# Kernel tuning notes

Measured on AMD Instinct MI355X. Metric: run time of the kernel, lower is better.

## Reference

```python
import jax, jax.numpy as jnp
import numpy as np

B, L, E, H = 8, 2048, 1024, 16
D = E // H
EPS = 1e-6


def setup_inputs() -> dict:
    key = jax.random.key(0)
    ks = jax.random.split(key, 9)
    s = 1.0 / np.sqrt(E)
    def lin_w(k):
        return jax.random.uniform(k, (E, E), jnp.float32, -s, s)
    def lin_b(k):
        return jax.random.uniform(k, (E,), jnp.float32, -s, s)
    return {
        "query": jax.random.normal(ks[0], (B, L, E), jnp.float32),
        "Wq": lin_w(ks[1]), "bq": lin_b(ks[2]),
        "Wk": lin_w(ks[3]), "bk": lin_b(ks[4]),
        "Wv": lin_w(ks[5]), "bv": lin_b(ks[6]),
        "Wo": lin_w(ks[7]), "bo": lin_b(ks[8]),
    }


def reference(query, Wq, bq, Wk, bk, Wv, bv, Wo, bo):
    bsz, tgt_len, embed_dim = query.shape
    n_head = H
    head_dim = embed_dim // n_head
    m = tgt_len  # src_len == tgt_len (self-attention)

    # projections (torch Linear with W stored as (in, out) here)
    q = query @ Wq + bq
    k = query @ Wk + bk
    v = query @ Wv + bv

    # (B, L, E) -> (B, H, L, D), softmax feature map over head dim
    def to_heads(x):
        return x.reshape(bsz, tgt_len, n_head, head_dim).transpose(0, 2, 1, 3)

    q = jax.nn.softmax(to_heads(q), axis=-1)
    k = jax.nn.softmax(to_heads(k), axis=-1)
    v = to_heads(v)
    comp_q = 1.0 - q
    comp_k = 1.0 - k

    # cosFormer positional reweighting: idx = (pi/2) * (1..m) / m
    idx = (np.pi / 2) * jnp.arange(1, m + 1, dtype=jnp.float32) / m  # (L,)
    sin = jnp.sin(idx)[None, None, :, None]  # (1,1,L,1)
    cos = jnp.cos(idx)[None, None, :, None]

    def feat(x):  # (B,H,L,D) -> (B,H,L,2D)
        return jnp.concatenate([x * sin, x * cos], axis=-1)

    qf, comp_qf = feat(q), feat(comp_q)
    kf, comp_kf = feat(k), feat(comp_k)

    def branch(qf_, kf_):
        kv = jnp.einsum('bhld,bhlm->bhdm', kf_, v)            # (B,H,2D,D)
        z = 1.0 / jnp.maximum(
            jnp.einsum('bhld,bhd->bhl', qf_, kf_.sum(axis=2)), EPS)
        return jnp.einsum('bhld,bhdm,bhl->bhlm', qf_, kv, z)  # (B,H,L,D)

    attn = branch(qf, kf) + branch(comp_qf, comp_kf)

    # torch: (B*H,L,D).transpose(0,1).view(L,B,E)
    out = attn.transpose(2, 0, 1, 3).reshape(tgt_len, bsz, embed_dim)
    out = out @ Wo + bo
    # torch final: .view(bsz, tgt_len, n_feat) -- raw reshape, no transpose
    return out.reshape(bsz, tgt_len, embed_dim)
```

## Files before the change

### kernel.cpp

```cpp
#include <hip/hip_runtime.h>
#include <hip/hip_bf16.h>
#include <cstdint>

#define B_   8
#define L_   2048
#define E_   1024
#define H_   16
#define D_   64
#define M_   (B_ * L_)
#define EPS_ 1e-6f
#define PI2_ 1.57079632679f

typedef __bf16 bf16;
typedef __bf16 bf16x8 __attribute__((ext_vector_type(8)));
typedef __bf16 bf16x4 __attribute__((ext_vector_type(4)));
typedef float  floatx4 __attribute__((ext_vector_type(4)));

__device__ inline void async_cp16(const void* g, void* l) {
  __builtin_amdgcn_global_load_lds(
      (__attribute__((address_space(1))) void*)const_cast<void*>(g),
      (__attribute__((address_space(3))) void*)l,
      16, 0, 0);
}

__global__ __launch_bounds__(256) void k_convert_x(const float* __restrict__ x,
                                                   bf16* __restrict__ o) {
  size_t i = ((size_t)blockIdx.x * 256 + threadIdx.x) * 8;
  floatx4 a = *(const floatx4*)(x + i);
  floatx4 b = *(const floatx4*)(x + i + 4);
  bf16x8 r;
  r[0] = (bf16)a[0]; r[1] = (bf16)a[1]; r[2] = (bf16)a[2]; r[3] = (bf16)a[3];
  r[4] = (bf16)b[0]; r[5] = (bf16)b[1]; r[6] = (bf16)b[2]; r[7] = (bf16)b[3];
  *(bf16x8*)(o + i) = r;
}

struct TArgs { const float* src[4]; bf16* dst[4]; };

__global__ __launch_bounds__(256) void k_transpose_w(TArgs t) {
  __shared__ float tile[32][33];
  const float* src = t.src[blockIdx.z];
  bf16* dst = t.dst[blockIdx.z];
  int bx = blockIdx.x, by = blockIdx.y;
  int x = threadIdx.x, y = threadIdx.y;
#pragma unroll
  for (int i = 0; i < 4; i++) {
    int r = by * 32 + y + i * 8;
    tile[y + i * 8][x] = src[(size_t)r * E_ + bx * 32 + x];
  }
  __syncthreads();
#pragma unroll
  for (int i = 0; i < 4; i++) {
    int r = bx * 32 + y + i * 8;
    dst[(size_t)r * E_ + by * 32 + x] = (bf16)tile[x][y + i * 8];
  }
}

__global__ __launch_bounds__(256) void k_gemm_qkv(const bf16* __restrict__ A,
                                                  const bf16* __restrict__ Wt,
                                                  const float* __restrict__ bq,
                                                  const float* __restrict__ bk,
                                                  const float* __restrict__ bv,
                                                  float* __restrict__ QT,
                                                  float* __restrict__ KT,
                                                  bf16* __restrict__ VT) {
  __shared__ __attribute__((aligned(16))) bf16 As[128 * 32];
  __shared__ __attribute__((aligned(16))) bf16 Bs[128 * 32];
  const int id = blockIdx.x;
  const int bn = id & 7;
  const int q  = id >> 3;
  const int bm = q / 3;
  const int z  = q - bm * 3;
  const bf16* Bt = Wt + (size_t)z * E_ * E_;
  const float* bias = (z == 0) ? bq : (z == 1) ? bk : bv;

  const int tid  = threadIdx.x;
  const int wid  = tid >> 6;
  const int lane = tid & 63;
  const int quad = lane >> 4;
  const int l15  = lane & 15;
  const int wm   = wid >> 1, wn = wid & 1;

  const bf16* ga0 = A  + (size_t)(bm * 128 + wid * 32 + (lane >> 2)) * E_ + (lane & 3) * 8;
  const bf16* ga1 = ga0 + (size_t)16 * E_;
  const bf16* gb0 = Bt + (size_t)(bn * 128 + wid * 32 + (lane >> 2)) * E_ + (lane & 3) * 8;
  const bf16* gb1 = gb0 + (size_t)16 * E_;
  bf16* la = &As[wid * 1024];
  bf16* lb = &Bs[wid * 1024];

  floatx4 acc[4][4] = {};

  for (int kk = 0; kk < E_; kk += 32) {
    async_cp16(ga0, la);        async_cp16(ga1, la + 512);
    async_cp16(gb0, lb);        async_cp16(gb1, lb + 512);
    ga0 += 32; ga1 += 32; gb0 += 32; gb1 += 32;
    __syncthreads();
    bf16x8 af[4], bfm[4];
#pragma unroll
    for (int i = 0; i < 4; i++)
      af[i] = *(const bf16x8*)&As[(wm * 64 + i * 16 + l15) * 32 + quad * 8];
#pragma unroll
    for (int i = 0; i < 4; i++)
      bfm[i] = *(const bf16x8*)&Bs[(wn * 64 + i * 16 + l15) * 32 + quad * 8];
#pragma unroll
    for (int i = 0; i < 4; i++)
#pragma unroll
      for (int j = 0; j < 4; j++)
        acc[i][j] = __builtin_amdgcn_mfma_f32_16x16x32_bf16(af[i], bfm[j], acc[i][j], 0, 0, 0);
    __syncthreads();
  }

#pragma unroll
  for (int i = 0; i < 4; i++)
#pragma unroll
    for (int j = 0; j < 4; j++) {
      const int c  = bn * 128 + wn * 64 + j * 16 + l15;
      const int r0 = bm * 128 + wm * 64 + i * 16 + quad * 4;
      const int h = c >> 6, d = c & 63;
      const int b = r0 >> 11, l = r0 & 2047;
      const float bv_ = bias[c];
      floatx4 v = acc[i][j];
      v[0] += bv_; v[1] += bv_; v[2] += bv_; v[3] += bv_;
      if (z == 0) {
        *(floatx4*)&QT[(((size_t)(b * 16 + h) * 64 + d) * 2048) + l] = v;
      } else if (z == 1) {
        *(floatx4*)&KT[(((size_t)(b * 16 + h) * 64 + d) * 2048) + l] = v;
      } else {
        bf16x4 r; r[0] = (bf16)v[0]; r[1] = (bf16)v[1]; r[2] = (bf16)v[2]; r[3] = (bf16)v[3];
        *(bf16x4*)&VT[(((size_t)(b * 16 + h) * 64 + d) * 2048) + l] = r;
      }
    }
}

#define AST 40
__global__ __launch_bounds__(256) void k_kv(const float* __restrict__ KT,
                                            const bf16* __restrict__ VT,
                                            float* __restrict__ kvp) {
  __shared__ __attribute__((aligned(16))) float kt[64 * 32];
  __shared__ __attribute__((aligned(16))) bf16  vt[64 * 32];
  __shared__ __attribute__((aligned(16))) bf16  Abuf[128 * AST];
  const int kseg = blockIdx.x;
  const int bh   = blockIdx.y;
  const int t = threadIdx.x;
  const int wid = t >> 6, lane = t & 63;
  const int quad = lane >> 4, l15 = lane & 15;
  const int wm = wid >> 1, wn = wid & 1;
  const int c = t >> 3, ii = t & 7;

  const float* ktg = KT + (size_t)bh * 64 * 2048;
  const bf16*  vtg = VT + (size_t)bh * 64 * 2048;

  floatx4 acc[4][2] = {};
  float rs = 0.f;

  for (int it = 0; it < 16; it++) {
    const int l0 = kseg * 512 + it * 32;
    {
      const int r = lane >> 3, ch = lane & 7;
      const float* g0 = ktg + (size_t)(wid * 16 + r) * 2048 + l0 + ch * 4;
      const float* g1 = ktg + (size_t)(wid * 16 + 8 + r) * 2048 + l0 + ch * 4;
      async_cp16(g0, &kt[(wid * 16) * 32]);
      async_cp16(g1, &kt[(wid * 16 + 8) * 32]);
    }
    {
      const int r = lane >> 2, ch = lane & 3;
      const bf16* g0 = vtg + (size_t)(wid * 16 + r) * 2048 + l0 + ch * 8;
      async_cp16(g0, &vt[(wid * 16) * 32]);
    }
    __syncthreads();

    float xv[8];
#pragma unroll
    for (int j = 0; j < 8; j++) xv[j] = kt[(ii + 8 * j) * 32 + c];
    float mx = xv[0];
#pragma unroll
    for (int j = 1; j < 8; j++) mx = fmaxf(mx, xv[j]);
    mx = fmaxf(mx, __shfl_xor(mx, 1));
    mx = fmaxf(mx, __shfl_xor(mx, 2));
    mx = fmaxf(mx, __shfl_xor(mx, 4));
    float s = 0.f;
#pragma unroll
    for (int j = 0; j < 8; j++) { xv[j] = __expf(xv[j] - mx); s += xv[j]; }
    s += __shfl_xor(s, 1); s += __shfl_xor(s, 2); s += __shfl_xor(s, 4);
    const float inv = 1.f / s;
    const int l = l0 + c;
    const float ang = PI2_ * (float)(l + 1) / (float)L_;
    const float sn = __sinf(ang), cs = __cosf(ang);
#pragma unroll
    for (int j = 0; j < 8; j++) {
      const float p = xv[j] * inv;
      const int f = ii + 8 * j;
      Abuf[f * AST + c]        = (bf16)(p * sn);
      Abuf[(64 + f) * AST + c] = (bf16)(p * cs);
    }
    __syncthreads();

    if (t < 128) {
      float r8 = 0.f;
#pragma unroll
      for (int g = 0; g < 4; g++) {
        bf16x8 v = *(const bf16x8*)&Abuf[t * AST + g * 8];
#pragma unroll
        for (int e = 0; e < 8; e++) r8 += (float)v[e];
      }
      rs += r8;
    }

    bf16x8 af[4], bfm[2];
#pragma unroll
    for (int i = 0; i < 4; i++)
      af[i] = *(const bf16x8*)&Abuf[(wm * 64 + i * 16 + l15) * AST + quad * 8];
#pragma unroll
    for (int j = 0; j < 2; j++)
      bfm[j] = *(const bf16x8*)&vt[(wn * 32 + j * 16 + l15) * 32 + quad * 8];
#pragma unroll
    for (int i = 0; i < 4; i++)
#pragma unroll
      for (int j = 0; j < 2; j++)
        acc[i][j] = __builtin_amdgcn_mfma_f32_16x16x32_bf16(af[i], bfm[j], acc[i][j], 0, 0, 0);
    __syncthreads();
  }

  float* C = kvp + (size_t)(kseg * 128 + bh) * 128 * 68;
#pragma unroll
  for (int i = 0; i < 4; i++)
#pragma unroll
    for (int j = 0; j < 2; j++) {
      const int col = wn * 32 + j * 16 + l15;
#pragma unroll
      for (int r = 0; r < 4; r++) {
        const int row = wm * 64 + i * 16 + quad * 4 + r;
        C[(size_t)row * 68 + col] = acc[i][j][r];
      }
    }
  if (t < 128) C[(size_t)t * 68 + 64] = rs;
}

__global__ __launch_bounds__(64) void k_consts(const float* __restrict__ kvp,
                                               bf16* __restrict__ KVT,
                                               float* __restrict__ ksbuf) {
  const int bh = blockIdx.x;
  const int dp = threadIdx.x;
  const size_t gs = (size_t)128 * 128 * 68;
  const float* P = kvp + (size_t)bh * 128 * 68;
  bf16* kr = KVT + (size_t)(bh * 64 + dp) * 160;
  float sk0 = 0.f, sk1 = 0.f;
#pragma unroll 8
  for (int f = 0; f < 128; f++) {
    float v = P[(size_t)f * 68 + dp] + P[gs + (size_t)f * 68 + dp]
            + P[2 * gs + (size_t)f * 68 + dp] + P[3 * gs + (size_t)f * 68 + dp];
    kr[f] = (bf16)v;
    if (f < 64) sk0 += v; else sk1 += v;
  }
  float ks0 = P[(size_t)dp * 68 + 64] + P[gs + (size_t)dp * 68 + 64]
            + P[2 * gs + (size_t)dp * 68 + 64] + P[3 * gs + (size_t)dp * 68 + 64];
  float ks1 = P[(size_t)(64 + dp) * 68 + 64] + P[gs + (size_t)(64 + dp) * 68 + 64]
            + P[2 * gs + (size_t)(64 + dp) * 68 + 64] + P[3 * gs + (size_t)(64 + dp) * 68 + 64];
  ksbuf[(size_t)bh * 136 + dp]      = ks0;
  ksbuf[(size_t)bh * 136 + 64 + dp] = ks1;
  float sks0 = ks0, sks1 = ks1;
#pragma unroll
  for (int o = 1; o < 64; o <<= 1) { sks0 += __shfl_xor(sks0, o); sks1 += __shfl_xor(sks1, o); }
  kr[128] = (bf16)(62.f * sk0);
  kr[129] = (bf16)(62.f * sk1);
#pragma unroll
  for (int f = 130; f < 160; f++) kr[f] = (bf16)0.f;
  if (dp == 0) {
    ksbuf[(size_t)bh * 136 + 128] = sks0;
    ksbuf[(size_t)bh * 136 + 129] = sks1;
  }
}

#define ASTR 168
__global__ __launch_bounds__(256) void k_attn(const float* __restrict__ QT,
                                              const bf16* __restrict__ KVT,
                                              const float* __restrict__ ksbuf,
                                              bf16* __restrict__ attn) {
  __shared__ __attribute__((aligned(16))) bf16 Abuf[128 * ASTR];
  __shared__ __attribute__((aligned(16))) bf16 Bbuf[64 * ASTR];
  __shared__ float ksl[136];
  const int lc = blockIdx.x;
  const int bh = blockIdx.y;
  const int b = bh >> 4, h = bh & 15;
  const int t = threadIdx.x;

  {
    const bf16* src = KVT + (size_t)bh * 64 * 160;
#pragma unroll
    for (int i = 0; i < 5; i++) {
      const int idx = t + i * 256;
      const int row = idx / 20, ch = idx % 20;
      *(bf16x8*)&Bbuf[row * ASTR + ch * 8] = *(const bf16x8*)(src + row * 160 + ch * 8);
    }
    if (t < 130) ksl[t] = ksbuf[(size_t)bh * 136 + t];
  }
  __syncthreads();

  if (t < 128) {
    const int l = lc * 128 + t;
    const float* qp = QT + ((size_t)bh * 64) * 2048 + l;
    float xv[64];
#pragma unroll
    for (int d = 0; d < 64; d++) xv[d] = qp[(size_t)d * 2048];
    float mx = -1e30f;
#pragma unroll
    for (int d = 0; d < 64; d++) mx = fmaxf(mx, xv[d]);
    float s = 0.f;
#pragma unroll
    for (int d = 0; d < 64; d++) { xv[d] = __expf(xv[d] - mx); s += xv[d]; }
    const float inv = 1.f / s;
    float t0 = 0.f, t1 = 0.f;
#pragma unroll
    for (int d = 0; d < 64; d++) {
      xv[d] *= inv;
      t0 += xv[d] * ksl[d];
      t1 += xv[d] * ksl[64 + d];
    }
    const float SKS0 = ksl[128], SKS1 = ksl[129];
    const float ang = PI2_ * (float)(l + 1) / (float)L_;
    const float sn = __sinf(ang), cs = __cosf(ang);
    const float den1 = sn * t0 + cs * t1;
    const float den2 = sn * (62.f * SKS0 + t0) + cs * (62.f * SKS1 + t1);
    const float z1 = 1.f / fmaxf(den1, EPS_);
    const float z2 = 1.f / fmaxf(den2, EPS_);
    const float zz = z1 + z2;
    const float a0 = zz * sn, a1 = zz * cs;
    bf16* ar = &Abuf[t * ASTR];
#pragma unroll
    for (int g = 0; g < 8; g++) {
      bf16x8 w;
#pragma unroll
      for (int j = 0; j < 8; j++) w[j] = (bf16)(a0 * xv[g * 8 + j]);
      *(bf16x8*)(ar + g * 8) = w;
    }
#pragma unroll
    for (int g = 0; g < 8; g++) {
      bf16x8 w;
#pragma unroll
      for (int j = 0; j < 8; j++) w[j] = (bf16)(a1 * xv[g * 8 + j]);
      *(bf16x8*)(ar + 64 + g * 8) = w;
    }
    bf16x8 wt = {};
    wt[0] = (bf16)(z2 * sn); wt[1] = (bf16)(z2 * cs);
    *(bf16x8*)(ar + 128) = wt;
    bf16x8 zr = {};
    *(bf16x8*)(ar + 136) = zr;
    *(bf16x8*)(ar + 144) = zr;
    *(bf16x8*)(ar + 152) = zr;
  }
  __syncthreads();

  const int wid = t >> 6, lane = t & 63;
  const int quad = lane >> 4, l15 = lane & 15;
  const int wm = wid >> 1, wn = wid & 1;
  floatx4 acc[4][2] = {};
#pragma unroll
  for (int kk = 0; kk < 5; kk++) {
    bf16x8 af[4], bfm[2];
#pragma unroll
    for (int i = 0; i < 4; i++)
      af[i] = *(const bf16x8*)&Abuf[(wm * 64 + i * 16 + l15) * ASTR + kk * 32 + quad * 8];
#pragma unroll
    for (int j = 0; j < 2; j++)
      bfm[j] = *(const bf16x8*)&Bbuf[(wn * 32 + j * 16 + l15) * ASTR + kk * 32 + quad * 8];
#pragma unroll
    for (int i = 0; i < 4; i++)
#pragma unroll
      for (int j = 0; j < 2; j++)
        acc[i][j] = __builtin_amdgcn_mfma_f32_16x16x32_bf16(af[i], bfm[j], acc[i][j], 0, 0, 0);
  }
#pragma unroll
  for (int i = 0; i < 4; i++)
#pragma unroll
    for (int j = 0; j < 2; j++) {
      const int dp = wn * 32 + j * 16 + l15;
#pragma unroll
      for (int r = 0; r < 4; r++) {
        const int l = lc * 128 + wm * 64 + i * 16 + quad * 4 + r;
        attn[((size_t)l * B_ + b) * E_ + h * 64 + dp] = (bf16)acc[i][j][r];
      }
    }
}

__global__ __launch_bounds__(256) void k_gemm_final(const bf16* __restrict__ A,
                                                    const bf16* __restrict__ Bt,
                                                    const float* __restrict__ bias,
                                                    float* __restrict__ C) {
  __shared__ __attribute__((aligned(16))) bf16 As[128 * 32];
  __shared__ __attribute__((aligned(16))) bf16 Bs[128 * 32];
  const int tid  = threadIdx.x;
  const int wid  = tid >> 6;
  const int lane = tid & 63;
  const int quad = lane >> 4;
  const int l15  = lane & 15;
  const int wm   = wid >> 1, wn = wid & 1;
  const int bm   = blockIdx.y, bn = blockIdx.x;

  const bf16* ga0 = A  + (size_t)(bm * 128 + wid * 32 + (lane >> 2)) * E_ + (lane & 3) * 8;
  const bf16* ga1 = ga0 + (size_t)16 * E_;
  const bf16* gb0 = Bt + (size_t)(bn * 128 + wid * 32 + (lane >> 2)) * E_ + (lane & 3) * 8;
  const bf16* gb1 = gb0 + (size_t)16 * E_;
  bf16* la = &As[wid * 1024];
  bf16* lb = &Bs[wid * 1024];

  floatx4 acc[4][4] = {};
  for (int kk = 0; kk < E_; kk += 32) {
    async_cp16(ga0, la);        async_cp16(ga1, la + 512);
    async_cp16(gb0, lb);        async_cp16(gb1, lb + 512);
    ga0 += 32; ga1 += 32; gb0 += 32; gb1 += 32;
    __syncthreads();
    bf16x8 af[4], bfm[4];
#pragma unroll
    for (int i = 0; i < 4; i++)
      af[i] = *(const bf16x8*)&As[(wm * 64 + i * 16 + l15) * 32 + quad * 8];
#pragma unroll
    for (int i = 0; i < 4; i++)
      bfm[i] = *(const bf16x8*)&Bs[(wn * 64 + i * 16 + l15) * 32 + quad * 8];
#pragma unroll
    for (int i = 0; i < 4; i++)
#pragma unroll
      for (int j = 0; j < 4; j++)
        acc[i][j] = __builtin_amdgcn_mfma_f32_16x16x32_bf16(af[i], bfm[j], acc[i][j], 0, 0, 0);
    __syncthreads();
  }
#pragma unroll
  for (int i = 0; i < 4; i++)
#pragma unroll
    for (int j = 0; j < 4; j++) {
      const int col = bn * 128 + wn * 64 + j * 16 + l15;
      const float bv = bias[col];
#pragma unroll
      for (int r = 0; r < 4; r++) {
        const int row = bm * 128 + wm * 64 + i * 16 + quad * 4 + r;
        C[(size_t)row * E_ + col] = acc[i][j][r] + bv;
      }
    }
}

extern "C" void kernel_launch(void* const* d_in, const int* in_sizes, int n_in,
                              void* d_out, int out_size, void* d_ws, size_t ws_size,
                              hipStream_t stream) {
  (void)in_sizes; (void)n_in; (void)out_size; (void)ws_size;
  const float* query = (const float*)d_in[0];
  const float* Wq = (const float*)d_in[1];
  const float* bq = (const float*)d_in[2];
  const float* Wk = (const float*)d_in[3];
  const float* bk = (const float*)d_in[4];
  const float* Wv = (const float*)d_in[5];
  const float* bv = (const float*)d_in[6];
  const float* Wo = (const float*)d_in[7];
  const float* bo = (const float*)d_in[8];

  char* ws = (char*)d_ws;
  float* QT   = (float*)(ws + 0);
  float* KT   = (float*)(ws + 67108864);
  bf16*  VT   = (bf16*) (ws + 134217728);
  bf16*  Wt   = (bf16*) (ws + 167772160);
  bf16*  Xbf  = (bf16*) (ws + 176160768);
  bf16*  attnb= (bf16*) (ws + 176160768);
  float* kvp  = (float*)(ws + 209715200);
  bf16*  KVT  = (bf16*) (ws + 227540992);
  float* ksbuf= (float*)(ws + 230162432);

  k_convert_x<<<(M_ * E_) / (256 * 8), 256, 0, stream>>>(query, Xbf);

  TArgs ta;
  ta.src[0] = Wq; ta.src[1] = Wk; ta.src[2] = Wv; ta.src[3] = Wo;
  ta.dst[0] = Wt;                       ta.dst[1] = Wt + (size_t)E_ * E_;
  ta.dst[2] = Wt + (size_t)2 * E_ * E_; ta.dst[3] = Wt + (size_t)3 * E_ * E_;
  k_transpose_w<<<dim3(32, 32, 4), dim3(32, 8), 0, stream>>>(ta);

  k_gemm_qkv<<<3072, 256, 0, stream>>>(Xbf, Wt, bq, bk, bv, QT, KT, VT);

  k_kv<<<dim3(4, 128), 256, 0, stream>>>(KT, VT, kvp);

  k_consts<<<128, 64, 0, stream>>>(kvp, KVT, ksbuf);

  k_attn<<<dim3(16, 128), 256, 0, stream>>>(QT, KVT, ksbuf, attnb);

  k_gemm_final<<<dim3(8, M_ / 128), 256, 0, stream>>>(attnb, Wt + (size_t)3 * E_ * E_, bo, (float*)d_out);
}
```

Before: 397.8 us.

## Replace QKV and output GEMMs with 256x256 pipelined double-buffered MFMA kernel

Both projection GEMMs move from 128x128 tiles with synchronous per-step loads to a shared 256x256-tile core with 8 waves, K-step 64, double-buffered LDS staging with async global->LDS copies interleaved with MFMA quarter-tiles, XOR-swizzled LDS columns, and s_setprio around MFMA bursts. Block IDs are remapped so that consecutive row tiles land on the same XCD for L2 reuse. This targets global/LDS traffic and the load latency that was exposed behind barriers in the GEMMs, which dominate runtime. It relies on hand-placed waitcnt/barrier sequences, which are fragile, and uses much larger register and LDS footprints.

```diff
diff --git a/kernel.cpp b/kernel.cpp
--- a/kernel.cpp
+++ b/kernel.cpp
@@ -55,78 +55,186 @@
   }
 }
 
-__global__ __launch_bounds__(256) void k_gemm_qkv(const bf16* __restrict__ A,
-                                                  const bf16* __restrict__ Wt,
-                                                  const float* __restrict__ bq,
-                                                  const float* __restrict__ bk,
-                                                  const float* __restrict__ bv,
-                                                  float* __restrict__ QT,
-                                                  float* __restrict__ KT,
-                                                  bf16* __restrict__ VT) {
-  __shared__ __attribute__((aligned(16))) bf16 As[128 * 32];
-  __shared__ __attribute__((aligned(16))) bf16 Bs[128 * 32];
-  const int id = blockIdx.x;
-  const int bn = id & 7;
-  const int q  = id >> 3;
-  const int bm = q / 3;
-  const int z  = q - bm * 3;
-  const bf16* Bt = Wt + (size_t)z * E_ * E_;
-  const float* bias = (z == 0) ? bq : (z == 1) ? bk : bv;
-
+#define BAR()   asm volatile("s_barrier" ::: "memory")
+#define LGKM0() asm volatile("s_waitcnt lgkmcnt(0)" ::: "memory")
+#define VMW4()  asm volatile("s_waitcnt vmcnt(4)" ::: "memory")
+#define VMW0()  asm volatile("s_waitcnt vmcnt(0)" ::: "memory")
+#define MFMA_   __builtin_amdgcn_mfma_f32_16x16x32_bf16
+
+#define GEMM_TILE(t_, c_) {                                                    \
+    const int t = (t_); const int c = (c_);                                    \
+    bf16x8 a0[4][2], a1[4][2], b0[2][2], b1[2][2];                             \
+                                                                  \
+    _Pragma("unroll") for (int i = 0; i < 4; i++) {                            \
+      a0[i][0] = RDA(c, 0, i); a0[i][1] = RDA(c, 1, i); }                      \
+    _Pragma("unroll") for (int j = 0; j < 2; j++) {                            \
+      b0[j][0] = RDB(c, 0, j); b0[j][1] = RDB(c, 1, j); }                      \
+    if (t + 1 < 16) STAGE(c ^ 1, 0, t + 1, 0);                                 \
+    BAR(); LGKM0();                                                            \
+    __builtin_amdgcn_s_setprio(1);                                             \
+    _Pragma("unroll") for (int i = 0; i < 4; i++)                              \
+      _Pragma("unroll") for (int j = 0; j < 2; j++) {                          \
+        acc[i][j] = MFMA_(a0[i][0], b0[j][0], acc[i][j], 0, 0, 0);             \
+        acc[i][j] = MFMA_(a0[i][1], b0[j][1], acc[i][j], 0, 0, 0); }           \
+    __builtin_amdgcn_s_setprio(0);                                             \
+    BAR();                                                                     \
+                                                                  \
+    _Pragma("unroll") for (int j = 0; j < 2; j++) {                            \
+      b1[j][0] = RDB(c, 0, j + 2); b1[j][1] = RDB(c, 1, j + 2); }              \
+    if (t + 1 < 16) STAGE(c ^ 1, 0, t + 1, 1);                                 \
+    BAR(); LGKM0();                                                            \
+    __builtin_amdgcn_s_setprio(1);                                             \
+    _Pragma("unroll") for (int i = 0; i < 4; i++)                              \
+      _Pragma("unroll") for (int j = 0; j < 2; j++) {                          \
+        acc[i][j + 2] = MFMA_(a0[i][0], b1[j][0], acc[i][j + 2], 0, 0, 0);     \
+        acc[i][j + 2] = MFMA_(a0[i][1], b1[j][1], acc[i][j + 2], 0, 0, 0); }   \
+    __builtin_amdgcn_s_setprio(0);                                             \
+    BAR();                                                                     \
+                                                                  \
+    _Pragma("unroll") for (int i = 0; i < 4; i++) {                            \
+      a1[i][0] = RDA(c, 0, i + 4); a1[i][1] = RDA(c, 1, i + 4); }              \
+    if (t + 2 < 16) STAGE(c, 1, t + 2, 0);                                     \
+    BAR(); LGKM0();                                                            \
+    __builtin_amdgcn_s_setprio(1);                                             \
+    _Pragma("unroll") for (int i = 0; i < 4; i++)                              \
+      _Pragma("unroll") for (int j = 0; j < 2; j++) {                          \
+        acc[i + 4][j + 2] = MFMA_(a1[i][0], b1[j][0], acc[i + 4][j + 2], 0, 0, 0); \
+        acc[i + 4][j + 2] = MFMA_(a1[i][1], b1[j][1], acc[i + 4][j + 2], 0, 0, 0); } \
+    __builtin_amdgcn_s_setprio(0);                                             \
+    BAR();                                                                     \
+                                                                  \
+    if (t < 14) { STAGE(c, 1, t + 2, 1); VMW4(); } else { VMW0(); }            \
+    BAR();                                                                     \
+    __builtin_amdgcn_s_setprio(1);                                             \
+    _Pragma("unroll") for (int i = 0; i < 4; i++)                              \
+      _Pragma("unroll") for (int j = 0; j < 2; j++) {                          \
+        acc[i + 4][j] = MFMA_(a1[i][0], b0[j][0], acc[i + 4][j], 0, 0, 0);     \
+        acc[i + 4][j] = MFMA_(a1[i][1], b0[j][1], acc[i + 4][j], 0, 0, 0); }   \
+    __builtin_amdgcn_s_setprio(0);                                             \
+    BAR();                                                                     \
+  }
+
+__device__ __forceinline__ void gemm256_core(const bf16* __restrict__ Agl,
+                                             const bf16* __restrict__ Bgl,
+                                             int bm, int bn, bf16* ldsb,
+                                             floatx4 (&acc)[8][4]) {
   const int tid  = threadIdx.x;
   const int wid  = tid >> 6;
   const int lane = tid & 63;
   const int quad = lane >> 4;
   const int l15  = lane & 15;
-  const int wm   = wid >> 1, wn = wid & 1;
-
-  const bf16* ga0 = A  + (size_t)(bm * 128 + wid * 32 + (lane >> 2)) * E_ + (lane & 3) * 8;
-  const bf16* ga1 = ga0 + (size_t)16 * E_;
-  const bf16* gb0 = Bt + (size_t)(bn * 128 + wid * 32 + (lane >> 2)) * E_ + (lane & 3) * 8;
-  const bf16* gb1 = gb0 + (size_t)16 * E_;
-  bf16* la = &As[wid * 1024];
-  bf16* lb = &Bs[wid * 1024];
-
-  floatx4 acc[4][4] = {};
-
-  for (int kk = 0; kk < E_; kk += 32) {
-    async_cp16(ga0, la);        async_cp16(ga1, la + 512);
-    async_cp16(gb0, lb);        async_cp16(gb1, lb + 512);
-    ga0 += 32; ga1 += 32; gb0 += 32; gb1 += 32;
-    __syncthreads();
-    bf16x8 af[4], bfm[4];
-#pragma unroll
-    for (int i = 0; i < 4; i++)
-      af[i] = *(const bf16x8*)&As[(wm * 64 + i * 16 + l15) * 32 + quad * 8];
-#pragma unroll
-    for (int i = 0; i < 4; i++)
-      bfm[i] = *(const bf16x8*)&Bs[(wn * 64 + i * 16 + l15) * 32 + quad * 8];
-#pragma unroll
-    for (int i = 0; i < 4; i++)
-#pragma unroll
-      for (int j = 0; j < 4; j++)
-        acc[i][j] = __builtin_amdgcn_mfma_f32_16x16x32_bf16(af[i], bfm[j], acc[i][j], 0, 0, 0);
-    __syncthreads();
-  }
-
-#pragma unroll
-  for (int i = 0; i < 4; i++)
+  const int wm   = wid >> 2;
+  const int wn   = wid & 3;
+  const int rb   = wn * 32;
+  const int gcol = wm * 32 + (((lane & 3) * 8) ^ ((lane & 32) ? 16 : 0));
+  const bf16* pA = Agl + (size_t)(bm * 256 + rb + (lane >> 2)) * E_ + gcol;
+  const bf16* pB = Bgl + (size_t)(bn * 256 + rb + (lane >> 2)) * E_ + gcol;
+  const int aCol = (quad * 8) ^ ((l15 & 8) ? 16 : 0);
+
+  auto LDSP = [&](int c, int mat, int qq, int row, int col) -> bf16* {
+    return ldsb + ((((c * 2 + mat) * 2 + qq) * 256 + row) * 32 + col);
+  };
+  auto STAGE = [&](int c, int mat, int tt, int h) {
+    const bf16* g = (mat ? pB : pA) + (size_t)(h * 128) * E_ + tt * 64;
+    bf16* lp = LDSP(c, mat, wm, h * 128 + rb, 0);
+    async_cp16(g, lp);
+    async_cp16(g + (size_t)16 * E_, lp + 16 * 32);
+  };
+  auto RDA = [&](int c, int qq, int i) -> bf16x8 {
+    return *(const bf16x8*)LDSP(c, 0, qq, wm * 128 + i * 16 + l15, aCol);
+  };
+  auto RDB = [&](int c, int qq, int j) -> bf16x8 {
+    return *(const bf16x8*)LDSP(c, 1, qq, wn * 64 + j * 16 + l15, aCol);
+  };
+
+  STAGE(0, 1, 0, 0); STAGE(0, 1, 0, 1);
+  STAGE(0, 0, 0, 0); STAGE(0, 0, 0, 1);
+  STAGE(1, 1, 1, 0); STAGE(1, 1, 1, 1);
+  VMW4();
+  BAR();
+
+#pragma unroll 1
+  for (int tb = 0; tb < 16; tb += 2) {
+    GEMM_TILE(tb, 0)
+    GEMM_TILE(tb + 1, 1)
+  }
+}
+
+__global__ __launch_bounds__(512, 2) void k_gemm_qkv256(
+    const bf16* __restrict__ A, const bf16* __restrict__ Wt,
+    const float* __restrict__ bq, const float* __restrict__ bk,
+    const float* __restrict__ bv,
+    float* __restrict__ QT, float* __restrict__ KT, bf16* __restrict__ VT) {
+  __shared__ __attribute__((aligned(16))) bf16 ldsb[2 * 2 * 2 * 256 * 32];
+  const int id  = blockIdx.x;
+  const int xcd = id & 7, rr = id >> 3;
+  const int bm  = xcd * 8 + rr / 12;
+  const int cz  = rr % 12;
+  const int bn  = cz & 3, z = cz >> 2;
+  const bf16* Bgl = Wt + (size_t)z * E_ * E_;
+
+  floatx4 acc[8][4] = {};
+  gemm256_core(A, Bgl, bm, bn, ldsb, acc);
+
+  const int tid  = threadIdx.x;
+  const int wid  = tid >> 6;
+  const int lane = tid & 63;
+  const int quad = lane >> 4;
+  const int l15  = lane & 15;
+  const int wm   = wid >> 2, wn = wid & 3;
+  const float* bias = (z == 0) ? bq : (z == 1) ? bk : bv;
+#pragma unroll
+  for (int i = 0; i < 8; i++)
 #pragma unroll
     for (int j = 0; j < 4; j++) {
-      const int c  = bn * 128 + wn * 64 + j * 16 + l15;
-      const int r0 = bm * 128 + wm * 64 + i * 16 + quad * 4;
-      const int h = c >> 6, d = c & 63;
-      const int b = r0 >> 11, l = r0 & 2047;
-      const float bv_ = bias[c];
+      const int col  = bn * 256 + wn * 64 + j * 16 + l15;
+      const int row0 = bm * 256 + wm * 128 + i * 16 + quad * 4;
+      const int h = col >> 6, d = col & 63;
+      const int b = row0 >> 11, l = row0 & 2047;
+      const float bb = bias[col];
       floatx4 v = acc[i][j];
-      v[0] += bv_; v[1] += bv_; v[2] += bv_; v[3] += bv_;
+      v[0] += bb; v[1] += bb; v[2] += bb; v[3] += bb;
       if (z == 0) {
         *(floatx4*)&QT[(((size_t)(b * 16 + h) * 64 + d) * 2048) + l] = v;
       } else if (z == 1) {
         *(floatx4*)&KT[(((size_t)(b * 16 + h) * 64 + d) * 2048) + l] = v;
       } else {
-        bf16x4 r; r[0] = (bf16)v[0]; r[1] = (bf16)v[1]; r[2] = (bf16)v[2]; r[3] = (bf16)v[3];
-        *(bf16x4*)&VT[(((size_t)(b * 16 + h) * 64 + d) * 2048) + l] = r;
+        bf16x4 rv;
+        rv[0] = (bf16)v[0]; rv[1] = (bf16)v[1];
+        rv[2] = (bf16)v[2]; rv[3] = (bf16)v[3];
+        *(bf16x4*)&VT[(((size_t)(b * 16 + h) * 64 + d) * 2048) + l] = rv;
+      }
+    }
+}
+
+__global__ __launch_bounds__(512, 2) void k_gemm_final256(
+    const bf16* __restrict__ A, const bf16* __restrict__ Bt,
+    const float* __restrict__ bias, float* __restrict__ C) {
+  __shared__ __attribute__((aligned(16))) bf16 ldsb[2 * 2 * 2 * 256 * 32];
+  const int id  = blockIdx.x;
+  const int xcd = id & 7, rr = id >> 3;
+  const int bm  = xcd * 8 + (rr >> 2);
+  const int bn  = rr & 3;
+
+  floatx4 acc[8][4] = {};
+  gemm256_core(A, Bt, bm, bn, ldsb, acc);
+
+  const int tid  = threadIdx.x;
+  const int wid  = tid >> 6;
+  const int lane = tid & 63;
+  const int quad = lane >> 4;
+  const int l15  = lane & 15;
+  const int wm   = wid >> 2, wn = wid & 3;
+#pragma unroll
+  for (int i = 0; i < 8; i++)
+#pragma unroll
+    for (int j = 0; j < 4; j++) {
+      const int col = bn * 256 + wn * 64 + j * 16 + l15;
+      const float bb = bias[col];
+#pragma unroll
+      for (int r = 0; r < 4; r++) {
+        const int row = bm * 256 + wm * 128 + i * 16 + quad * 4 + r;
+        C[(size_t)row * E_ + col] = acc[i][j][r] + bb;
       }
     }
 }
@@ -381,61 +489,6 @@
     }
 }
 
-__global__ __launch_bounds__(256) void k_gemm_final(const bf16* __restrict__ A,
-                                                    const bf16* __restrict__ Bt,
-                                                    const float* __restrict__ bias,
-                                                    float* __restrict__ C) {
-  __shared__ __attribute__((aligned(16))) bf16 As[128 * 32];
-  __shared__ __attribute__((aligned(16))) bf16 Bs[128 * 32];
-  const int tid  = threadIdx.x;
-  const int wid  = tid >> 6;
-  const int lane = tid & 63;
-  const int quad = lane >> 4;
-  const int l15  = lane & 15;
-  const int wm   = wid >> 1, wn = wid & 1;
-  const int bm   = blockIdx.y, bn = blockIdx.x;
-
-  const bf16* ga0 = A  + (size_t)(bm * 128 + wid * 32 + (lane >> 2)) * E_ + (lane & 3) * 8;
-  const bf16* ga1 = ga0 + (size_t)16 * E_;
-  const bf16* gb0 = Bt + (size_t)(bn * 128 + wid * 32 + (lane >> 2)) * E_ + (lane & 3) * 8;
-  const bf16* gb1 = gb0 + (size_t)16 * E_;
-  bf16* la = &As[wid * 1024];
-  bf16* lb = &Bs[wid * 1024];
-
-  floatx4 acc[4][4] = {};
-  for (int kk = 0; kk < E_; kk += 32) {
-    async_cp16(ga0, la);        async_cp16(ga1, la + 512);
-    async_cp16(gb0, lb);        async_cp16(gb1, lb + 512);
-    ga0 += 32; ga1 += 32; gb0 += 32; gb1 += 32;
-    __syncthreads();
-    bf16x8 af[4], bfm[4];
-#pragma unroll
-    for (int i = 0; i < 4; i++)
-      af[i] = *(const bf16x8*)&As[(wm * 64 + i * 16 + l15) * 32 + quad * 8];
-#pragma unroll
-    for (int i = 0; i < 4; i++)
-      bfm[i] = *(const bf16x8*)&Bs[(wn * 64 + i * 16 + l15) * 32 + quad * 8];
-#pragma unroll
-    for (int i = 0; i < 4; i++)
-#pragma unroll
-      for (int j = 0; j < 4; j++)
-        acc[i][j] = __builtin_amdgcn_mfma_f32_16x16x32_bf16(af[i], bfm[j], acc[i][j], 0, 0, 0);
-    __syncthreads();
-  }
-#pragma unroll
-  for (int i = 0; i < 4; i++)
-#pragma unroll
-    for (int j = 0; j < 4; j++) {
-      const int col = bn * 128 + wn * 64 + j * 16 + l15;
-      const float bv = bias[col];
-#pragma unroll
-      for (int r = 0; r < 4; r++) {
-        const int row = bm * 128 + wm * 64 + i * 16 + quad * 4 + r;
-        C[(size_t)row * E_ + col] = acc[i][j][r] + bv;
-      }
-    }
-}
-
 extern "C" void kernel_launch(void* const* d_in, const int* in_sizes, int n_in,
                               void* d_out, int out_size, void* d_ws, size_t ws_size,
                               hipStream_t stream) {
@@ -469,7 +522,7 @@
   ta.dst[2] = Wt + (size_t)2 * E_ * E_; ta.dst[3] = Wt + (size_t)3 * E_ * E_;
   k_transpose_w<<<dim3(32, 32, 4), dim3(32, 8), 0, stream>>>(ta);
 
-  k_gemm_qkv<<<3072, 256, 0, stream>>>(Xbf, Wt, bq, bk, bv, QT, KT, VT);
+  k_gemm_qkv256<<<768, 512, 0, stream>>>(Xbf, Wt, bq, bk, bv, QT, KT, VT);
 
   k_kv<<<dim3(4, 128), 256, 0, stream>>>(KT, VT, kvp);
 
@@ -477,5 +530,5 @@
 
   k_attn<<<dim3(16, 128), 256, 0, stream>>>(QT, KVT, ksbuf, attnb);
 
-  k_gemm_final<<<dim3(8, M_ / 128), 256, 0, stream>>>(attnb, Wt + (size_t)3 * E_ * E_, bo, (float*)d_out);
-}
+  k_gemm_final256<<<256, 512, 0, stream>>>(attnb, Wt + (size_t)3 * E_ * E_, bo, (float*)d_out);
+}
```

Result: faster. 362.8 us (-8.8%).
